# Kernel optimization log

Measured on AMD Instinct MI355X. Metric: run time of the kernel, lower is better.

## Reference

```python
import jax, jax.numpy as jnp
import numpy as np

BLOCK = 128        # block_size in the source
FP8_MAX = 448.0    # float8_e4m3 max magnitude


def act_quant(x):
    """Per-token, per-128-column block activation quantization (fp8 simulate).
    x: [T, K] -> (x_q [T, K], scale [T, K//BLOCK])"""
    T, K = x.shape
    xb = x.reshape(T, K // BLOCK, BLOCK)
    s = jnp.max(jnp.abs(xb), axis=-1, keepdims=True) / FP8_MAX  # [T, K/B, 1]
    s = jnp.maximum(s, jnp.asarray(1e-12, x.dtype))
    xq = jnp.clip(xb / s, -FP8_MAX, FP8_MAX)
    return xq, s  # keep blocked shapes


def weight_dequant(wq, scale):
    """Dequantize weight with per-128x128-block scales.
    wq: [N, K], scale: [N//BLOCK, K//BLOCK] -> [N, K]"""
    N, K = wq.shape
    wb = wq.reshape(N // BLOCK, BLOCK, K // BLOCK, BLOCK)
    return (wb * scale[:, None, :, None]).reshape(N, K)


def reference(x, weight_q, w_scale, bias):
    # fp8 branch of linear(): act_quant -> fp8_gemm (dequant both sides) -> bias add
    T, K = x.shape
    xq, xs = act_quant(x)                       # [T,K/B,B], [T,K/B,1]
    x_deq = (xq * xs).reshape(T, K)             # dequantized activations
    w_deq = weight_dequant(weight_q, w_scale)   # [N, K]
    y = jnp.einsum('tk,nk->tn', x_deq, w_deq) + bias
    return y


def setup_inputs() -> dict:
    key = jax.random.key(0)
    k1, k2, k3, k4 = jax.random.split(key, 4)
    T, K, N = 8192, 4096, 4096
    x = jax.random.normal(k1, (T, K), dtype=jnp.float32)
    weight_q = jax.random.normal(k2, (N, K), dtype=jnp.float32)
    w_scale = jax.random.uniform(k3, (N // BLOCK, K // BLOCK), dtype=jnp.float32)
    bias = jax.random.normal(k4, (N,), dtype=jnp.float32)
    return {"x": x, "weight_q": weight_q, "w_scale": w_scale, "bias": bias}
```

## Files before the change

### kernel.cpp

```cpp
#include <hip/hip_runtime.h>
#include <hip/hip_bf16.h>
#include <stdint.h>

typedef __bf16 bf16_t;
typedef __bf16 bf16x8 __attribute__((ext_vector_type(8)));
typedef float f32x4 __attribute__((ext_vector_type(4)));
typedef unsigned int u32;

__device__ __forceinline__ void async_copy16(void* lds, const void* gmem) {
    __builtin_amdgcn_global_load_lds(
        (const __attribute__((address_space(1))) u32*)gmem,
        (__attribute__((address_space(3))) u32*)lds, 16, 0, 0);
}

#define BAR() do { asm volatile("" ::: "memory"); \
                   __builtin_amdgcn_s_barrier();  \
                   asm volatile("" ::: "memory"); } while (0)
#define VMCNT(N) asm volatile("s_waitcnt vmcnt(" #N ")" ::: "memory")

__global__ void cvt_x_kernel(const float* __restrict__ in,
                             bf16_t* __restrict__ out, int n8) {
    int stride = gridDim.x * blockDim.x;
    for (int i = blockIdx.x * blockDim.x + threadIdx.x; i < n8; i += stride) {
        const float4* p = (const float4*)in + 2 * (size_t)i;
        float4 a = p[0], b = p[1];
        bf16x8 o;
        o[0] = (__bf16)a.x; o[1] = (__bf16)a.y; o[2] = (__bf16)a.z; o[3] = (__bf16)a.w;
        o[4] = (__bf16)b.x; o[5] = (__bf16)b.y; o[6] = (__bf16)b.z; o[7] = (__bf16)b.w;
        *(bf16x8*)(out + 8 * (size_t)i) = o;
    }
}

__global__ void cvt_w_kernel(const float* __restrict__ w,
                             const float* __restrict__ wsc,
                             bf16_t* __restrict__ out, int n8, int K, int KB) {
    int stride = gridDim.x * blockDim.x;
    for (int i = blockIdx.x * blockDim.x + threadIdx.x; i < n8; i += stride) {
        int e = i * 8;
        int row = e / K;
        int col = e - row * K;
        float s = wsc[(row >> 7) * KB + (col >> 7)];
        const float4* p = (const float4*)w + 2 * (size_t)i;
        float4 a = p[0], b = p[1];
        bf16x8 o;
        o[0] = (__bf16)(a.x * s); o[1] = (__bf16)(a.y * s);
        o[2] = (__bf16)(a.z * s); o[3] = (__bf16)(a.w * s);
        o[4] = (__bf16)(b.x * s); o[5] = (__bf16)(b.y * s);
        o[6] = (__bf16)(b.z * s); o[7] = (__bf16)(b.w * s);
        *(bf16x8*)(out + 8 * (size_t)i) = o;
    }
}

__global__ __launch_bounds__(512, 2) void gemm256_8ph(
    const bf16_t* __restrict__ A,
    const bf16_t* __restrict__ B,
    const float* __restrict__ bias,
    float* __restrict__ C,
    int M, int N, int K, int tiles_n) {
    __shared__ __attribute__((aligned(16))) char smem[131072];

    const int tid = threadIdx.x;
    const int lane = tid & 63;
    const int wv = tid >> 6;
    const int wr = wv >> 2;
    const int wc = wv & 3;
    const int la = lane & 15;
    const int hi = lane >> 4;

    const int nwg = gridDim.x;
    int wg = blockIdx.x;
    if ((nwg & 7) == 0) wg = (wg & 7) * (nwg >> 3) + (wg >> 3);
    const int tm = wg / tiles_n, tn = wg % tiles_n;

    const long arow = (long)tm * 256;
    const long bcol = (long)tn * 256;

    const int srow = tid >> 3;
    const int scolb = ((tid & 7) * 16) ^ ((tid & 32) ? 32 : 0);
    const size_t rstep = (size_t)K * 2;
    const char* pa = (const char*)A + (size_t)(arow + srow) * rstep + scolb;
    const char* pb = (const char*)B + (size_t)(bcol + srow) * rstep + scolb;
    char* const lb = (char*)smem;
    const int ldst = tid * 16;

    const int swz = (lane & 4) << 3;
    const int aoff = (((wr * 128 + la) * 128) + hi * 16) ^ swz;
    const int boff = (((wc * 64 + la) * 128) + hi * 16) ^ swz;

#define STAGE_A(BUF, H, KT) do { \
        const char* _s = pa + (size_t)(KT) * 128 + (size_t)(H) * 128 * rstep; \
        char* _d = lb + (BUF) * 65536 + (H) * 16384 + ldst; \
        async_copy16(_d, _s); \
        async_copy16(_d + 8192, _s + 64 * rstep); \
    } while (0)
#define STAGE_B(BUF, H, KT) do { \
        const char* _s = pb + (size_t)(KT) * 128 + (size_t)(H) * 128 * rstep; \
        char* _d = lb + (BUF) * 65536 + 32768 + (H) * 16384 + ldst; \
        async_copy16(_d, _s); \
        async_copy16(_d + 8192, _s + 64 * rstep); \
    } while (0)
#define RD_A(BUF, MM, KS) (*(const bf16x8*)(lb + (BUF) * 65536 + (aoff + (MM) * 2048 + (KS) * 64)))
#define RD_B(BUF, NN, KS) (*(const bf16x8*)(lb + (BUF) * 65536 + 32768 + (boff + (NN) * 2048 + (KS) * 64)))

    f32x4 acc[8][4];
#pragma unroll
    for (int m = 0; m < 8; ++m)
#pragma unroll
        for (int n = 0; n < 4; ++n) {
            f32x4 z = {0.f, 0.f, 0.f, 0.f};
            acc[m][n] = z;
        }
    bf16x8 a[4][2], b0[2][2], b1[2][2];

    const int nt = K >> 6;

    STAGE_A(0, 0, 0); STAGE_A(0, 1, 0);
    STAGE_B(0, 0, 0); STAGE_B(0, 1, 0);
    STAGE_B(1, 0, 1); STAGE_B(1, 1, 1);
    VMCNT(4);
    BAR();

    for (int kt = 0; kt < nt; kt += 2) {
#define KTILE(CUR, KTV) do { \
        const int _ktA = ((KTV) + 1 < nt) ? (KTV) + 1 : nt - 1; \
        const int _ktB = ((KTV) + 2 < nt) ? (KTV) + 2 : nt - 1; \
         \
        _Pragma("unroll") for (int m = 0; m < 4; ++m) { a[m][0] = RD_A(CUR, m, 0); a[m][1] = RD_A(CUR, m, 1); } \
        _Pragma("unroll") for (int n = 0; n < 2; ++n) { b0[n][0] = RD_B(CUR, n, 0); b0[n][1] = RD_B(CUR, n, 1); } \
        STAGE_A((CUR) ^ 1, 0, _ktA); \
        BAR(); \
        __builtin_amdgcn_s_setprio(1); \
        _Pragma("unroll") for (int ks = 0; ks < 2; ++ks) \
            _Pragma("unroll") for (int m = 0; m < 4; ++m) \
                _Pragma("unroll") for (int n = 0; n < 2; ++n) \
                    acc[m][n] = __builtin_amdgcn_mfma_f32_16x16x32_bf16(a[m][ks], b0[n][ks], acc[m][n], 0, 0, 0); \
        __builtin_amdgcn_s_setprio(0); \
        BAR(); \
         \
        _Pragma("unroll") for (int n = 0; n < 2; ++n) { b1[n][0] = RD_B(CUR, 2 + n, 0); b1[n][1] = RD_B(CUR, 2 + n, 1); } \
        STAGE_A((CUR) ^ 1, 1, _ktA); \
        BAR(); \
        __builtin_amdgcn_s_setprio(1); \
        _Pragma("unroll") for (int ks = 0; ks < 2; ++ks) \
            _Pragma("unroll") for (int m = 0; m < 4; ++m) \
                _Pragma("unroll") for (int n = 0; n < 2; ++n) \
                    acc[m][2 + n] = __builtin_amdgcn_mfma_f32_16x16x32_bf16(a[m][ks], b1[n][ks], acc[m][2 + n], 0, 0, 0); \
        __builtin_amdgcn_s_setprio(0); \
        BAR(); \
         \
        _Pragma("unroll") for (int m = 0; m < 4; ++m) { a[m][0] = RD_A(CUR, 4 + m, 0); a[m][1] = RD_A(CUR, 4 + m, 1); } \
        STAGE_B(CUR, 0, _ktB); \
        BAR(); \
        __builtin_amdgcn_s_setprio(1); \
        _Pragma("unroll") for (int ks = 0; ks < 2; ++ks) \
            _Pragma("unroll") for (int m = 0; m < 4; ++m) \
                _Pragma("unroll") for (int n = 0; n < 2; ++n) \
                    acc[4 + m][2 + n] = __builtin_amdgcn_mfma_f32_16x16x32_bf16(a[m][ks], b1[n][ks], acc[4 + m][2 + n], 0, 0, 0); \
        __builtin_amdgcn_s_setprio(0); \
        BAR(); \
         \
        STAGE_B(CUR, 1, _ktB); \
        BAR(); \
        __builtin_amdgcn_s_setprio(1); \
        _Pragma("unroll") for (int ks = 0; ks < 2; ++ks) \
            _Pragma("unroll") for (int m = 0; m < 4; ++m) \
                _Pragma("unroll") for (int n = 0; n < 2; ++n) \
                    acc[4 + m][n] = __builtin_amdgcn_mfma_f32_16x16x32_bf16(a[m][ks], b0[n][ks], acc[4 + m][n], 0, 0, 0); \
        __builtin_amdgcn_s_setprio(0); \
        VMCNT(4); \
        BAR(); \
    } while (0)
        KTILE(0, kt);
        KTILE(1, kt + 1);
#undef KTILE
    }

    const float* bp = bias + bcol + wc * 64 + la;
    const float bv0 = bp[0], bv1 = bp[16], bv2 = bp[32], bv3 = bp[48];
    float* cbase = C + (arow + wr * 128 + hi * 4) * (long)N + bcol + wc * 64 + la;
#pragma unroll
    for (int m = 0; m < 8; ++m)
#pragma unroll
        for (int r = 0; r < 4; ++r) {
            float* cp = cbase + (size_t)(m * 16 + r) * N;
            cp[0]  = acc[m][0][r] + bv0;
            cp[16] = acc[m][1][r] + bv1;
            cp[32] = acc[m][2][r] + bv2;
            cp[48] = acc[m][3][r] + bv3;
        }
#undef STAGE_A
#undef STAGE_B
#undef RD_A
#undef RD_B
}

__global__ __launch_bounds__(256) void gemm_bt_bias(
    const bf16_t* __restrict__ A, const bf16_t* __restrict__ B,
    const float* __restrict__ bias, float* __restrict__ C,
    int M, int N, int K) {
    __shared__ bf16_t As[128 * 32];
    __shared__ bf16_t Bs[128 * 32];
    const int t = threadIdx.x;
    const int lane = t & 63;
    const int wave = t >> 6;
    const int wr = wave >> 1, wc = wave & 1;
    const long arow = (long)blockIdx.y * 128;
    const long bcol = (long)blockIdx.x * 128;
    const int r0 = t >> 2, c0 = (t & 3) * 8;
    const bf16_t* Ag = A + (arow + r0) * K + c0;
    const bf16_t* Bg = B + (bcol + r0) * K + c0;
    bf16_t* Al = As + t * 8;
    bf16_t* Bl = Bs + t * 8;
    const size_t gstep = (size_t)64 * K;
    f32x4 acc[4][4];
#pragma unroll
    for (int m = 0; m < 4; ++m)
#pragma unroll
        for (int n = 0; n < 4; ++n) { f32x4 z = {0.f,0.f,0.f,0.f}; acc[m][n] = z; }
    const int la = lane & 15, kg = (lane >> 4) * 8;
    for (int k0 = 0; k0 < K; k0 += 32) {
        async_copy16(Al, Ag + k0);        async_copy16(Al + 2048, Ag + k0 + gstep);
        async_copy16(Bl, Bg + k0);        async_copy16(Bl + 2048, Bg + k0 + gstep);
        __syncthreads();
        bf16x8 af[4], bfv[4];
#pragma unroll
        for (int m = 0; m < 4; ++m) af[m]  = *(const bf16x8*)(As + (wr*64 + m*16 + la)*32 + kg);
#pragma unroll
        for (int n = 0; n < 4; ++n) bfv[n] = *(const bf16x8*)(Bs + (wc*64 + n*16 + la)*32 + kg);
#pragma unroll
        for (int m = 0; m < 4; ++m)
#pragma unroll
            for (int n = 0; n < 4; ++n)
                acc[m][n] = __builtin_amdgcn_mfma_f32_16x16x32_bf16(af[m], bfv[n], acc[m][n], 0,0,0);
        __syncthreads();
    }
    const int lg = lane >> 4;
#pragma unroll
    for (int n = 0; n < 4; ++n) {
        const long col = bcol + wc * 64 + n * 16 + la;
        const float bv = bias[col];
#pragma unroll
        for (int m = 0; m < 4; ++m) {
            const long row = arow + wr * 64 + m * 16 + lg * 4;
            float* cp = C + row * (long)N + col;
#pragma unroll
            for (int r = 0; r < 4; ++r) cp[(size_t)r * N] = acc[m][n][r] + bv;
        }
    }
}

__global__ void naive_kernel(const float* __restrict__ x, const float* __restrict__ w,
                             const float* __restrict__ wsc, const float* __restrict__ bias,
                             float* __restrict__ out, int T, int N, int K, int KB) {
    long i = (long)blockIdx.x * blockDim.x + threadIdx.x;
    if (i >= (long)T * N) return;
    int tt = (int)(i / N), n = (int)(i % N);
    float accum = 0.f;
    for (int kb = 0; kb < KB; ++kb) {
        float s = wsc[(n >> 7) * KB + kb];
        float p = 0.f;
        const float* xp = x + (long)tt * K + kb * 128;
        const float* wp = w + (long)n * K + kb * 128;
        for (int k = 0; k < 128; ++k) p += xp[k] * wp[k];
        accum += p * s;
    }
    out[i] = accum + bias[n];
}

extern "C" void kernel_launch(void* const* d_in, const int* in_sizes, int n_in,
                              void* d_out, int out_size, void* d_ws, size_t ws_size,
                              hipStream_t stream) {
    const float* x    = (const float*)d_in[0];
    const float* wq   = (const float*)d_in[1];
    const float* wsc  = (const float*)d_in[2];
    const float* bias = (const float*)d_in[3];
    float* out = (float*)d_out;

    const int N = in_sizes[3];
    const int K = in_sizes[1] / N;
    const int T = in_sizes[0] / K;
    const int KB = K / 128;

    const size_t need = ((size_t)T * K + (size_t)N * K) * sizeof(bf16_t);
    const bool t256 = (T % 256 == 0) && (N % 256 == 0) && (K % 128 == 0) && (K >= 128);
    const bool t128 = (T % 128 == 0) && (N % 128 == 0) && (K % 32 == 0) && (K % 128 == 0);

    if (ws_size < need || (!t256 && !t128)) {
        long total = (long)T * N;
        naive_kernel<<<(int)((total + 255) / 256), 256, 0, stream>>>(
            x, wq, wsc, bias, out, T, N, K, KB);
        return;
    }

    bf16_t* xb = (bf16_t*)d_ws;
    bf16_t* wb = xb + (size_t)T * K;

    cvt_x_kernel<<<2048, 256, 0, stream>>>(x, xb, T * (K / 8));
    cvt_w_kernel<<<2048, 256, 0, stream>>>(wq, wsc, wb, N * (K / 8), K, KB);

    if (t256) {
        const int tiles_n = N / 256;
        const int nwg = (T / 256) * tiles_n;
        gemm256_8ph<<<nwg, 512, 0, stream>>>(xb, wb, bias, out, T, N, K, tiles_n);
    } else {
        dim3 grid(N / 128, T / 128);
        gemm_bt_bias<<<grid, 256, 0, stream>>>(xb, wb, bias, out, T, N, K);
    }
}
```

Baseline: 497.6 us.

## Fuse conversion kernels and widen LDS XOR swizzle in GEMM

Merges the x and weight fp32-to-bf16 conversion kernels into a single grid-stride launch that uses nontemporal loads, removing one launch and the gap between the two. It also changes the LDS swizzle from a single-bit XOR to a 3-bit row-based XOR across 16-byte chunks, applied consistently to the async stage writes and the fragment reads, to cut LDS bank conflicts in the GEMM. The fused kernel adds a branch per element, and the new swizzle has to stay consistent with the rest of the unshown kernel code.

```diff
diff --git a/kernel.cpp b/kernel.cpp
--- a/kernel.cpp
+++ b/kernel.cpp
@@ -18,36 +18,38 @@
                    asm volatile("" ::: "memory"); } while (0)
 #define VMCNT(N) asm volatile("s_waitcnt vmcnt(" #N ")" ::: "memory")
 
-__global__ void cvt_x_kernel(const float* __restrict__ in,
-                             bf16_t* __restrict__ out, int n8) {
+__global__ void cvt_fused(const float* __restrict__ x,
+                          const float* __restrict__ w,
+                          const float* __restrict__ wsc,
+                          bf16_t* __restrict__ xb, bf16_t* __restrict__ wb,
+                          int nx8, int nw8, int K, int KB) {
     int stride = gridDim.x * blockDim.x;
-    for (int i = blockIdx.x * blockDim.x + threadIdx.x; i < n8; i += stride) {
-        const float4* p = (const float4*)in + 2 * (size_t)i;
-        float4 a = p[0], b = p[1];
-        bf16x8 o;
-        o[0] = (__bf16)a.x; o[1] = (__bf16)a.y; o[2] = (__bf16)a.z; o[3] = (__bf16)a.w;
-        o[4] = (__bf16)b.x; o[5] = (__bf16)b.y; o[6] = (__bf16)b.z; o[7] = (__bf16)b.w;
-        *(bf16x8*)(out + 8 * (size_t)i) = o;
-    }
-}
-
-__global__ void cvt_w_kernel(const float* __restrict__ w,
-                             const float* __restrict__ wsc,
-                             bf16_t* __restrict__ out, int n8, int K, int KB) {
-    int stride = gridDim.x * blockDim.x;
-    for (int i = blockIdx.x * blockDim.x + threadIdx.x; i < n8; i += stride) {
-        int e = i * 8;
-        int row = e / K;
-        int col = e - row * K;
-        float s = wsc[(row >> 7) * KB + (col >> 7)];
-        const float4* p = (const float4*)w + 2 * (size_t)i;
-        float4 a = p[0], b = p[1];
-        bf16x8 o;
-        o[0] = (__bf16)(a.x * s); o[1] = (__bf16)(a.y * s);
-        o[2] = (__bf16)(a.z * s); o[3] = (__bf16)(a.w * s);
-        o[4] = (__bf16)(b.x * s); o[5] = (__bf16)(b.y * s);
-        o[6] = (__bf16)(b.z * s); o[7] = (__bf16)(b.w * s);
-        *(bf16x8*)(out + 8 * (size_t)i) = o;
+    int ntot = nx8 + nw8;
+    for (int i = blockIdx.x * blockDim.x + threadIdx.x; i < ntot; i += stride) {
+        if (i < nx8) {
+            const f32x4* p = (const f32x4*)x + 2 * (size_t)i;
+            f32x4 a = __builtin_nontemporal_load(p);
+            f32x4 b = __builtin_nontemporal_load(p + 1);
+            bf16x8 o;
+            o[0] = (__bf16)a[0]; o[1] = (__bf16)a[1]; o[2] = (__bf16)a[2]; o[3] = (__bf16)a[3];
+            o[4] = (__bf16)b[0]; o[5] = (__bf16)b[1]; o[6] = (__bf16)b[2]; o[7] = (__bf16)b[3];
+            *(bf16x8*)(xb + 8 * (size_t)i) = o;
+        } else {
+            int j = i - nx8;
+            int e = j * 8;
+            int row = e / K;
+            int col = e - row * K;
+            float s = wsc[(row >> 7) * KB + (col >> 7)];
+            const f32x4* p = (const f32x4*)w + 2 * (size_t)j;
+            f32x4 a = __builtin_nontemporal_load(p);
+            f32x4 b = __builtin_nontemporal_load(p + 1);
+            bf16x8 o;
+            o[0] = (__bf16)(a[0] * s); o[1] = (__bf16)(a[1] * s);
+            o[2] = (__bf16)(a[2] * s); o[3] = (__bf16)(a[3] * s);
+            o[4] = (__bf16)(b[0] * s); o[5] = (__bf16)(b[1] * s);
+            o[6] = (__bf16)(b[2] * s); o[7] = (__bf16)(b[3] * s);
+            *(bf16x8*)(wb + 8 * (size_t)j) = o;
+        }
     }
 }
 
@@ -76,16 +78,18 @@
     const long bcol = (long)tn * 256;
 
     const int srow = tid >> 3;
-    const int scolb = ((tid & 7) * 16) ^ ((tid & 32) ? 32 : 0);
+    const int scolb = ((tid & 7) * 16) ^ (((tid >> 3) & 7) << 4);
     const size_t rstep = (size_t)K * 2;
     const char* pa = (const char*)A + (size_t)(arow + srow) * rstep + scolb;
     const char* pb = (const char*)B + (size_t)(bcol + srow) * rstep + scolb;
     char* const lb = (char*)smem;
     const int ldst = tid * 16;
 
-    const int swz = (lane & 4) << 3;
-    const int aoff = (((wr * 128 + la) * 128) + hi * 16) ^ swz;
-    const int boff = (((wc * 64 + la) * 128) + hi * 16) ^ swz;
+    const int swz = (la & 7) << 4;
+    const int cb0 = (hi * 16) ^ swz;
+    const int cb1 = cb0 ^ 64;
+    const int arowoff = (wr * 128 + la) * 128;
+    const int browoff = 32768 + (wc * 64 + la) * 128;
 
 #define STAGE_A(BUF, H, KT) do { \
         const char* _s = pa + (size_t)(KT) * 128 + (size_t)(H) * 128 * rstep; \
@@ -99,8 +103,8 @@
         async_copy16(_d, _s); \
         async_copy16(_d + 8192, _s + 64 * rstep); \
     } while (0)
-#define RD_A(BUF, MM, KS) (*(const bf16x8*)(lb + (BUF) * 65536 + (aoff + (MM) * 2048 + (KS) * 64)))
-#define RD_B(BUF, NN, KS) (*(const bf16x8*)(lb + (BUF) * 65536 + 32768 + (boff + (NN) * 2048 + (KS) * 64)))
+#define RD_A(BUF, MM, CB) (*(const bf16x8*)(lb + (BUF) * 65536 + arowoff + (MM) * 2048 + (CB)))
+#define RD_B(BUF, NN, CB) (*(const bf16x8*)(lb + (BUF) * 65536 + browoff + (NN) * 2048 + (CB)))
 
     f32x4 acc[8][4];
 #pragma unroll
@@ -125,8 +129,8 @@
         const int _ktA = ((KTV) + 1 < nt) ? (KTV) + 1 : nt - 1; \
         const int _ktB = ((KTV) + 2 < nt) ? (KTV) + 2 : nt - 1; \
          \
-        _Pragma("unroll") for (int m = 0; m < 4; ++m) { a[m][0] = RD_A(CUR, m, 0); a[m][1] = RD_A(CUR, m, 1); } \
-        _Pragma("unroll") for (int n = 0; n < 2; ++n) { b0[n][0] = RD_B(CUR, n, 0); b0[n][1] = RD_B(CUR, n, 1); } \
+        _Pragma("unroll") for (int m = 0; m < 4; ++m) { a[m][0] = RD_A(CUR, m, cb0); a[m][1] = RD_A(CUR, m, cb1); } \
+        _Pragma("unroll") for (int n = 0; n < 2; ++n) { b0[n][0] = RD_B(CUR, n, cb0); b0[n][1] = RD_B(CUR, n, cb1); } \
         STAGE_A((CUR) ^ 1, 0, _ktA); \
         BAR(); \
         __builtin_amdgcn_s_setprio(1); \
@@ -137,7 +141,7 @@
         __builtin_amdgcn_s_setprio(0); \
         BAR(); \
          \
-        _Pragma("unroll") for (int n = 0; n < 2; ++n) { b1[n][0] = RD_B(CUR, 2 + n, 0); b1[n][1] = RD_B(CUR, 2 + n, 1); } \
+        _Pragma("unroll") for (int n = 0; n < 2; ++n) { b1[n][0] = RD_B(CUR, 2 + n, cb0); b1[n][1] = RD_B(CUR, 2 + n, cb1); } \
         STAGE_A((CUR) ^ 1, 1, _ktA); \
         BAR(); \
         __builtin_amdgcn_s_setprio(1); \
@@ -148,7 +152,7 @@
         __builtin_amdgcn_s_setprio(0); \
         BAR(); \
          \
-        _Pragma("unroll") for (int m = 0; m < 4; ++m) { a[m][0] = RD_A(CUR, 4 + m, 0); a[m][1] = RD_A(CUR, 4 + m, 1); } \
+        _Pragma("unroll") for (int m = 0; m < 4; ++m) { a[m][0] = RD_A(CUR, 4 + m, cb0); a[m][1] = RD_A(CUR, 4 + m, cb1); } \
         STAGE_B(CUR, 0, _ktB); \
         BAR(); \
         __builtin_amdgcn_s_setprio(1); \
@@ -295,8 +299,8 @@
     bf16_t* xb = (bf16_t*)d_ws;
     bf16_t* wb = xb + (size_t)T * K;
 
-    cvt_x_kernel<<<2048, 256, 0, stream>>>(x, xb, T * (K / 8));
-    cvt_w_kernel<<<2048, 256, 0, stream>>>(wq, wsc, wb, N * (K / 8), K, KB);
+    cvt_fused<<<2048, 256, 0, stream>>>(x, wq, wsc, xb, wb,
+                                        T * (K / 8), N * (K / 8), K, KB);
 
     if (t256) {
         const int tiles_n = N / 256;
```

Measured after the change: 463.2 us. 1.07x faster.
